# Performance work log

Hardware: AMD Instinct MI355X
Metric: run time of the kernel (lower is better)

## Reference

```python
import jax, jax.numpy as jnp
import numpy as np

N = 50000   # nodes
E = 800000  # edges
IN = 128
HID = 128
L = 4       # GraphConv layers
OUT = 47    # classes
EPS = 1e-5  # BatchNorm eps


def setup_inputs() -> dict:
    key = jax.random.key(0)
    ks = jax.random.split(key, 12)
    feat = jax.random.normal(ks[0], (N, IN), jnp.float32)
    src = jax.random.randint(ks[1], (E,), 0, N, jnp.int32)
    dst = jax.random.randint(ks[2], (E,), 0, N, jnp.int32)
    enc_W = jax.random.normal(ks[3], (L, IN, HID), jnp.float32) * 0.05
    enc_bias = jnp.zeros((HID,), jnp.float32)
    bn_gamma = jnp.ones((L, HID), jnp.float32)
    bn_beta = jnp.zeros((L, HID), jnp.float32)
    bn_mean = jax.random.normal(ks[4], (L, HID), jnp.float32) * 0.1
    bn_var = jnp.ones((L, HID), jnp.float32) + 0.1 * jax.random.uniform(ks[5], (L, HID), jnp.float32)
    cls_W0 = jax.random.normal(ks[6], (HID * L, HID), jnp.float32) * 0.05
    cls_b0 = jnp.zeros((HID,), jnp.float32)
    cls_gamma0 = jnp.ones((HID,), jnp.float32)
    cls_beta0 = jnp.zeros((HID,), jnp.float32)
    cls_mean0 = jax.random.normal(ks[7], (HID,), jnp.float32) * 0.1
    cls_var0 = jnp.ones((HID,), jnp.float32) + 0.1 * jax.random.uniform(ks[8], (HID,), jnp.float32)
    cls_W1 = jax.random.normal(ks[9], (HID, OUT), jnp.float32) * 0.05
    cls_b1 = jnp.zeros((OUT,), jnp.float32)
    return dict(feat=feat, src=src, dst=dst, enc_W=enc_W, enc_bias=enc_bias,
                bn_gamma=bn_gamma, bn_beta=bn_beta, bn_mean=bn_mean, bn_var=bn_var,
                cls_W0=cls_W0, cls_b0=cls_b0, cls_gamma0=cls_gamma0, cls_beta0=cls_beta0,
                cls_mean0=cls_mean0, cls_var0=cls_var0, cls_W1=cls_W1, cls_b1=cls_b1)


def _bn_eval(x, gamma, beta, mean, var):
    return (x - mean) * (gamma * jax.lax.rsqrt(var + EPS)) + beta


def reference(feat, src, dst, enc_W, enc_bias, bn_gamma, bn_beta, bn_mean, bn_var,
              cls_W0, cls_b0, cls_gamma0, cls_beta0, cls_mean0, cls_var0, cls_W1, cls_b1):
    ones = jnp.ones((E,), jnp.float32)
    out_deg = jnp.clip(jax.ops.segment_sum(ones, src, num_segments=N), 1.0)
    in_deg = jnp.clip(jax.ops.segment_sum(ones, dst, num_segments=N), 1.0)
    norm_src = jax.lax.rsqrt(out_deg)[:, None]  # [N,1]
    norm_dst = jax.lax.rsqrt(in_deg)[:, None]

    h = feat  # inference: dropout = identity
    feat_lst = []
    for i in range(L):
        # GraphConv 'both': D_out^{-1/2} pre-scale, XW, scatter-add over edges, D_in^{-1/2} post-scale
        hw = (h * norm_src) @ enc_W[i]                         # [N,HID]
        agg = jax.ops.segment_sum(hw[src], dst, num_segments=N)  # sparse neighbor aggregation
        h = agg * norm_dst
        if i == L - 1:  # only last GraphConv has bias
            h = h + enc_bias
        h = _bn_eval(h, bn_gamma[i], bn_beta[i], bn_mean[i], bn_var[i])
        h = jax.nn.relu(h)
        feat_lst.append(h)

    h = jnp.concatenate(feat_lst, axis=-1)  # JK concat -> [N, HID*L]
    # classifier layer 0: Linear + BN + ReLU (dropout off in eval)
    h = _bn_eval(h @ cls_W0 + cls_b0, cls_gamma0, cls_beta0, cls_mean0, cls_var0)
    h = jax.nn.relu(h)
    # classifier layer 1: Linear only
    return h @ cls_W1 + cls_b1  # [N, OUT]
```

## Files before the change

### kernel.cpp

```cpp
#include <hip/hip_runtime.h>
#include <hip/hip_bf16.h>
#include <hip/hip_fp16.h>

#define EPS 1e-5f
#define HB 128
#define HRANGE 25600
#define NN2 51200

typedef __attribute__((ext_vector_type(8))) short short8;
typedef __attribute__((ext_vector_type(4))) float f32x4;

__device__ __forceinline__ unsigned short f2bf_rn(float f) {
    unsigned u = __builtin_bit_cast(unsigned, f);
    u += 0x7fffu + ((u >> 16) & 1u);
    return (unsigned short)(u >> 16);
}
__device__ __forceinline__ float bf2f(unsigned short h) {
    return __builtin_bit_cast(float, (unsigned)h << 16);
}
__device__ __forceinline__ unsigned packsplit(float x) {
    unsigned short h = f2bf_rn(x);
    unsigned short l = f2bf_rn(x - bf2f(h));
    return ((unsigned)h << 16) | l;
}

__global__ __launch_bounds__(1024) void hist_kernel(
    const int* __restrict__ src, const int* __restrict__ dst,
    unsigned* __restrict__ histW, int E, int EperB) {
    __shared__ unsigned cnt[HRANGE];
    const int b = blockIdx.x, tid = threadIdx.x;
    const long e0 = (long)b * EperB;
    const long e1 = min(e0 + (long)EperB, (long)E);
    #pragma unroll 2
    for (int arr = 0; arr < 2; ++arr) {
        const int* a = arr ? src : dst;
        for (int j = tid; j < HRANGE; j += 1024) cnt[j] = 0;
        __syncthreads();
        for (long e = e0 + tid; e < e1; e += 1024) {
            int v = a[e];
            atomicAdd(&cnt[v >> 1], 1u << ((v & 1) << 4));
        }
        __syncthreads();
        unsigned* o = histW + ((size_t)(arr * HB + b)) * HRANGE;
        for (int j = tid; j < HRANGE; j += 1024) o[j] = cnt[j];
        __syncthreads();
    }
}

__global__ __launch_bounds__(256) void merge_kernel(
    const unsigned short* __restrict__ hist16, int* __restrict__ pdeg,
    unsigned short* __restrict__ bp16, float* __restrict__ nsrc,
    float* __restrict__ ndst, int N) {
    int n = blockIdx.x * blockDim.x + threadIdx.x;
    if (n >= NN2) return;
    unsigned s = 0;
    #pragma unroll 8
    for (int b = 0; b < HB; ++b) {
        unsigned c = hist16[(size_t)b * NN2 + n];
        bp16[(size_t)b * NN2 + n] = (unsigned short)s;
        s += c;
    }
    unsigned s2 = 0;
    #pragma unroll 8
    for (int b = 0; b < HB; ++b) s2 += hist16[(size_t)(HB + b) * NN2 + n];
    if (n < N) {
        pdeg[n] = (int)((s + 15u) & ~15u);
        ndst[n] = rsqrtf((float)max((int)s, 1));
        nsrc[n] = rsqrtf((float)max((int)s2, 1));
    }
}

__global__ __launch_bounds__(256) void scan_partial_kernel(const int* __restrict__ deg,
                                                           int* __restrict__ bsums, int n) {
    __shared__ int wsum[4];
    const int tid = threadIdx.x, lane = tid & 63, wid = tid >> 6;
    const int i0 = blockIdx.x * 1024 + tid * 4;
    int s = 0;
    if (i0 + 3 < n) {
        int4 v = *(const int4*)(deg + i0);
        s = v.x + v.y + v.z + v.w;
    } else {
        for (int j = 0; j < 4; ++j) if (i0 + j < n) s += deg[i0 + j];
    }
    #pragma unroll
    for (int off = 32; off >= 1; off >>= 1) s += __shfl_down(s, off, 64);
    if (lane == 0) wsum[wid] = s;
    __syncthreads();
    if (tid == 0) bsums[blockIdx.x] = wsum[0] + wsum[1] + wsum[2] + wsum[3];
}

__global__ __launch_bounds__(64) void scan_bsums_kernel(int* __restrict__ bsums,
                                                        int* __restrict__ offs, int nb, int n) {
    int lane = threadIdx.x;
    int v = (lane < nb) ? bsums[lane] : 0;
    int x = v;
    #pragma unroll
    for (int off = 1; off < 64; off <<= 1) {
        int t = __shfl_up(x, off, 64);
        if (lane >= off) x += t;
    }
    if (lane < nb) bsums[lane] = x - v;
    if (lane == 63) offs[n] = x;
}

__global__ __launch_bounds__(256) void scan_final_kernel(const int* __restrict__ deg,
                                                         const int* __restrict__ bsums,
                                                         int* __restrict__ offs, int n) {
    __shared__ int wsum[4];
    const int tid = threadIdx.x, lane = tid & 63, wid = tid >> 6;
    const int i0 = blockIdx.x * 1024 + tid * 4;
    int d0 = 0, d1 = 0, d2 = 0, d3 = 0;
    if (i0 + 3 < n) {
        int4 v = *(const int4*)(deg + i0);
        d0 = v.x; d1 = v.y; d2 = v.z; d3 = v.w;
    } else {
        if (i0 + 0 < n) d0 = deg[i0 + 0];
        if (i0 + 1 < n) d1 = deg[i0 + 1];
        if (i0 + 2 < n) d2 = deg[i0 + 2];
        if (i0 + 3 < n) d3 = deg[i0 + 3];
    }
    int s = d0 + d1 + d2 + d3;
    int x = s;
    #pragma unroll
    for (int off = 1; off < 64; off <<= 1) {
        int t = __shfl_up(x, off, 64);
        if (lane >= off) x += t;
    }
    if (lane == 63) wsum[wid] = x;
    __syncthreads();
    int wpre = 0;
    #pragma unroll
    for (int w = 0; w < 4; ++w) if (w < wid) wpre += wsum[w];
    int base = bsums[blockIdx.x] + wpre + (x - s);
    if (i0 + 0 < n) offs[i0 + 0] = base;
    if (i0 + 1 < n) offs[i0 + 1] = base + d0;
    if (i0 + 2 < n) offs[i0 + 2] = base + d0 + d1;
    if (i0 + 3 < n) offs[i0 + 3] = base + d0 + d1 + d2;
}

__global__ void fill_pad_kernel(int* __restrict__ csc, int total, int N) {
    int i = blockIdx.x * blockDim.x + threadIdx.x;
    int o = i * 4;
    if (o + 3 < total) {
        *(int4*)(csc + o) = make_int4(N, N, N, N);
    } else {
        for (int j = 0; j < 4 && o + j < total; ++j) csc[o + j] = N;
    }
}

__global__ __launch_bounds__(1024) void fill_kernel(
    const int* __restrict__ src, const int* __restrict__ dst,
    const int* __restrict__ offs, const unsigned short* __restrict__ bp16,
    int* __restrict__ csc, int E, int EperB) {
    __shared__ unsigned cur[HRANGE];
    const int b = blockIdx.x, tid = threadIdx.x;
    const long e0 = (long)b * EperB;
    const long e1 = min(e0 + (long)EperB, (long)E);
    for (int j = tid; j < HRANGE; j += 1024) cur[j] = 0;
    __syncthreads();
    const unsigned short* bprow = bp16 + (size_t)b * NN2;
    for (long e = e0 + tid; e < e1; e += 1024) {
        int d = dst[e];
        int sh = (d & 1) << 4;
        unsigned old = atomicAdd(&cur[d >> 1], 1u << sh);
        unsigned rank = (old >> sh) & 0xffffu;
        unsigned p = (unsigned)offs[d] + (unsigned)bprow[d] + rank;
        csc[p] = src[e];
    }
}

__device__ __forceinline__ void pack_frag(
    const float* __restrict__ B, short* __restrict__ hi, short* __restrict__ lo,
    int K, int NCF, int strideB, int ncols, int t) {
    int KF = K >> 5;
    int lane = t & 63;
    int fid = t >> 6;
    int cf = fid / KF;
    int kf = fid % KF;
    int col = cf * 16 + (lane & 15);
    int k0 = kf * 32 + (lane >> 4) * 8;
    int o = t * 8;
    #pragma unroll
    for (int j = 0; j < 8; ++j) {
        float x = (col < ncols) ? B[(size_t)(k0 + j) * strideB + col] : 0.f;
        unsigned short h = f2bf_rn(x);
        hi[o + j] = (short)h;
        lo[o + j] = (short)f2bf_rn(x - bf2f(h));
    }
}

__global__ __launch_bounds__(256) void pack_all_kernel(
    const float* __restrict__ enc_W, const float* __restrict__ cls_W0,
    const float* __restrict__ cls_W1,
    short* __restrict__ encBhi, short* __restrict__ encBlo,
    short* __restrict__ clsBhi, short* __restrict__ clsBlo,
    short* __restrict__ w1hi, short* __restrict__ w1lo) {
    int t = blockIdx.x * blockDim.x + threadIdx.x;
    if (t < 8192) {
        int i = t >> 11, tt = t & 2047;
        pack_frag(enc_W + (size_t)i * 128 * 128, encBhi + i * 16384, encBlo + i * 16384,
                  128, 8, 128, 128, tt);
    } else if (t < 16384) {
        pack_frag(cls_W0, clsBhi, clsBlo, 512, 8, 128, 128, t - 8192);
    } else if (t < 16384 + 768) {
        pack_frag(cls_W1, w1hi, w1lo, 128, 3, 47, 47, t - 16384);
    }
}

template<bool PACKED>
__global__ __launch_bounds__(256) void mfma_gemm_kernel(
    const void* __restrict__ Av, const short* __restrict__ Bhi, const short* __restrict__ Blo,
    const float* __restrict__ nsrc, __half* __restrict__ C, int M) {
    __shared__ short Bh_sh[16384];
    __shared__ short Bl_sh[16384];
    const int tid = threadIdx.x;
    const int lane = tid & 63;
    const int wid  = tid >> 6;
    const int row0 = blockIdx.x * 128 + wid * 32;
    const int rsub = lane & 15;
    const int kg   = lane >> 4;

    short8 ahi[2][4], alo[2][4];
    #pragma unroll
    for (int rf = 0; rf < 2; ++rf) {
        const int rowa = min(row0 + rf * 16 + rsub, M - 1);
        #pragma unroll
        for (int kf = 0; kf < 4; ++kf) {
            short8 h, l;
            if (PACKED) {
                const unsigned* ap = (const unsigned*)Av + (size_t)rowa * 128 + kg * 8;
                uint4 u0 = *(const uint4*)(ap + kf * 32);
                uint4 u1 = *(const uint4*)(ap + kf * 32 + 4);
                unsigned uu[8] = {u0.x, u0.y, u0.z, u0.w, u1.x, u1.y, u1.z, u1.w};
                #pragma unroll
                for (int j = 0; j < 8; ++j) {
                    h[j] = (short)(uu[j] >> 16);
                    l[j] = (short)(uu[j] & 0xffffu);
                }
            } else {
                const float* ap = (const float*)Av + (size_t)rowa * 128 + kg * 8;
                float4 v0 = *(const float4*)(ap + kf * 32);
                float4 v1 = *(const float4*)(ap + kf * 32 + 4);
                float v[8] = {v0.x, v0.y, v0.z, v0.w, v1.x, v1.y, v1.z, v1.w};
                #pragma unroll
                for (int j = 0; j < 8; ++j) {
                    unsigned short hb = f2bf_rn(v[j]);
                    h[j] = (short)hb;
                    l[j] = (short)f2bf_rn(v[j] - bf2f(hb));
                }
            }
            ahi[rf][kf] = h; alo[rf][kf] = l;
        }
    }

    #pragma unroll
    for (int i = 0; i < 8; ++i) {
        int o = (tid + i * 256) * 8;
        *(uint4*)&Bh_sh[o] = *(const uint4*)&Bhi[o];
        *(uint4*)&Bl_sh[o] = *(const uint4*)&Blo[o];
    }
    __syncthreads();

    f32x4 acc[2][8];
    #pragma unroll
    for (int rf = 0; rf < 2; ++rf)
        #pragma unroll
        for (int cf = 0; cf < 8; ++cf) acc[rf][cf] = (f32x4){0.f, 0.f, 0.f, 0.f};

    #pragma unroll
    for (int cf = 0; cf < 8; ++cf) {
        #pragma unroll
        for (int kf = 0; kf < 4; ++kf) {
            int o = ((cf * 4 + kf) * 64 + lane) * 8;
            short8 bh = *(const short8*)&Bh_sh[o];
            short8 bl = *(const short8*)&Bl_sh[o];
            #pragma unroll
            for (int rf = 0; rf < 2; ++rf) {
                acc[rf][cf] = __builtin_amdgcn_mfma_f32_16x16x32_bf16(ahi[rf][kf], bh, acc[rf][cf], 0, 0, 0);
                acc[rf][cf] = __builtin_amdgcn_mfma_f32_16x16x32_bf16(alo[rf][kf], bh, acc[rf][cf], 0, 0, 0);
                acc[rf][cf] = __builtin_amdgcn_mfma_f32_16x16x32_bf16(ahi[rf][kf], bl, acc[rf][cf], 0, 0, 0);
            }
        }
    }

    #pragma unroll
    for (int rf = 0; rf < 2; ++rf)
        #pragma unroll
        for (int r = 0; r < 4; ++r) {
            int row = row0 + rf * 16 + kg * 4 + r;
            if (row < M) {
                float sc = nsrc[row];
                __half* cp = C + (size_t)row * 128 + rsub;
                #pragma unroll
                for (int cf = 0; cf < 8; ++cf) cp[cf * 16] = __float2half(acc[rf][cf][r] * sc);
            }
        }
}

__global__ __launch_bounds__(256) void aggregate_kernel(
    const __half* __restrict__ hw, const int* __restrict__ offs, const int* __restrict__ csc,
    const float* __restrict__ norm_dst, const float* __restrict__ bias,
    const float* __restrict__ gamma, const float* __restrict__ beta,
    const float* __restrict__ mean, const float* __restrict__ var,
    unsigned* __restrict__ hout, int n) {
    const int lane = threadIdx.x & 63;
    const int gw = (blockIdx.x * blockDim.x + threadIdx.x) >> 6;
    const int nw = (gridDim.x * blockDim.x) >> 6;
    const int c = lane * 2;

    const float sc0 = gamma[c] * rsqrtf(var[c] + EPS);
    const float sc1 = gamma[c + 1] * rsqrtf(var[c + 1] + EPS);
    const float mn0 = mean[c], mn1 = mean[c + 1];
    const float bt0 = beta[c], bt1 = beta[c + 1];
    const float bi0 = bias ? bias[c] : 0.f;
    const float bi1 = bias ? bias[c + 1] : 0.f;

    for (int v = gw; v < n; v += nw) {
        const int e0 = offs[v], e1 = offs[v + 1];
        float2 acc = make_float2(0.f, 0.f);
        for (int e = e0; e < e1; e += 16) {
            int4 ca = *(const int4*)(csc + e);
            int4 cb = *(const int4*)(csc + e + 4);
            int4 cc = *(const int4*)(csc + e + 8);
            int4 cd = *(const int4*)(csc + e + 12);
            float2 p0 = __half22float2(*(const __half2*)(hw + (size_t)ca.x * 128 + c));
            float2 p1 = __half22float2(*(const __half2*)(hw + (size_t)ca.y * 128 + c));
            float2 p2 = __half22float2(*(const __half2*)(hw + (size_t)ca.z * 128 + c));
            float2 p3 = __half22float2(*(const __half2*)(hw + (size_t)ca.w * 128 + c));
            float2 p4 = __half22float2(*(const __half2*)(hw + (size_t)cb.x * 128 + c));
            float2 p5 = __half22float2(*(const __half2*)(hw + (size_t)cb.y * 128 + c));
            float2 p6 = __half22float2(*(const __half2*)(hw + (size_t)cb.z * 128 + c));
            float2 p7 = __half22float2(*(const __half2*)(hw + (size_t)cb.w * 128 + c));
            float2 p8 = __half22float2(*(const __half2*)(hw + (size_t)cc.x * 128 + c));
            float2 p9 = __half22float2(*(const __half2*)(hw + (size_t)cc.y * 128 + c));
            float2 pa = __half22float2(*(const __half2*)(hw + (size_t)cc.z * 128 + c));
            float2 pb = __half22float2(*(const __half2*)(hw + (size_t)cc.w * 128 + c));
            float2 pc = __half22float2(*(const __half2*)(hw + (size_t)cd.x * 128 + c));
            float2 pd = __half22float2(*(const __half2*)(hw + (size_t)cd.y * 128 + c));
            float2 pe = __half22float2(*(const __half2*)(hw + (size_t)cd.z * 128 + c));
            float2 pf = __half22float2(*(const __half2*)(hw + (size_t)cd.w * 128 + c));
            acc.x += (((p0.x + p1.x) + (p2.x + p3.x)) + ((p4.x + p5.x) + (p6.x + p7.x)))
                   + (((p8.x + p9.x) + (pa.x + pb.x)) + ((pc.x + pd.x) + (pe.x + pf.x)));
            acc.y += (((p0.y + p1.y) + (p2.y + p3.y)) + ((p4.y + p5.y) + (p6.y + p7.y)))
                   + (((p8.y + p9.y) + (pa.y + pb.y)) + ((pc.y + pd.y) + (pe.y + pf.y)));
        }
        float nd = norm_dst[v];
        float h0 = fmaxf((acc.x * nd + bi0 - mn0) * sc0 + bt0, 0.f);
        float h1 = fmaxf((acc.y * nd + bi1 - mn1) * sc1 + bt1, 0.f);
        uint2 w = make_uint2(packsplit(h0), packsplit(h1));
        *(uint2*)(hout + (size_t)v * 128 + c) = w;
    }
}

__global__ __launch_bounds__(256) void classifier_kernel(
    const unsigned* __restrict__ h1, const unsigned* __restrict__ h2,
    const unsigned* __restrict__ h3, const unsigned* __restrict__ h4,
    const short* __restrict__ Bhi, const short* __restrict__ Blo,
    const short* __restrict__ W1hi, const short* __restrict__ W1lo,
    const float* __restrict__ b0,
    const float* __restrict__ g, const float* __restrict__ bt,
    const float* __restrict__ mn, const float* __restrict__ vr,
    const float* __restrict__ b1,
    float* __restrict__ out, int M) {
    __shared__ short Bh_sh[2][4096];
    __shared__ short Bl_sh[2][4096];
    __shared__ unsigned zw[4][16 * 128];
    const int tid = threadIdx.x, lane = tid & 63, wid = tid >> 6;
    const int rsub = lane & 15;
    const int kg   = lane >> 4;
    const int row0 = blockIdx.x * 128 + wid * 32;
    const unsigned* hb[4] = {h1, h2, h3, h4};

    const int scf = tid >> 5, ssub = tid & 31;
    const int sl = scf * 512 + ssub * 16;

    float biasv[8], scalev[8], meanv[8], betav[8];
    #pragma unroll
    for (int cf = 0; cf < 8; ++cf) {
        int col = cf * 16 + rsub;
        biasv[cf] = b0[col];
        scalev[cf] = g[col] * rsqrtf(vr[col] + EPS);
        meanv[cf] = mn[col];
        betav[cf] = bt[col];
    }

    f32x4 acc[2][8];
    #pragma unroll
    for (int rf = 0; rf < 2; ++rf)
        #pragma unroll
        for (int cf = 0; cf < 8; ++cf) acc[rf][cf] = (f32x4){0.f, 0.f, 0.f, 0.f};

    {
        size_t goff = ((size_t)(scf * 16 + 0) * 64) * 8 + ssub * 16;
        *(uint4*)&Bh_sh[0][sl]     = *(const uint4*)&Bhi[goff];
        *(uint4*)&Bh_sh[0][sl + 8] = *(const uint4*)&Bhi[goff + 8];
        *(uint4*)&Bl_sh[0][sl]     = *(const uint4*)&Blo[goff];
        *(uint4*)&Bl_sh[0][sl + 8] = *(const uint4*)&Blo[goff + 8];
    }
    __syncthreads();

    const int rowa0 = min(row0 + rsub, M - 1);
    const int rowa1 = min(row0 + 16 + rsub, M - 1);

    for (int kf16 = 0; kf16 < 16; ++kf16) {
        const int cur = kf16 & 1;
        uint4 st0, st1, st2, st3;
        if (kf16 < 15) {
            size_t goff = ((size_t)(scf * 16 + kf16 + 1) * 64) * 8 + ssub * 16;
            st0 = *(const uint4*)&Bhi[goff];
            st1 = *(const uint4*)&Bhi[goff + 8];
            st2 = *(const uint4*)&Blo[goff];
            st3 = *(const uint4*)&Blo[goff + 8];
        }
        short8 ah[2], al[2];
        #pragma unroll
        for (int rf = 0; rf < 2; ++rf) {
            const unsigned* ap = hb[kf16 >> 2] + (size_t)(rf ? rowa1 : rowa0) * 128
                                 + (kf16 & 3) * 32 + kg * 8;
            uint4 u0 = *(const uint4*)(ap);
            uint4 u1 = *(const uint4*)(ap + 4);
            unsigned uu[8] = {u0.x, u0.y, u0.z, u0.w, u1.x, u1.y, u1.z, u1.w};
            #pragma unroll
            for (int j = 0; j < 8; ++j) {
                ah[rf][j] = (short)(uu[j] >> 16);
                al[rf][j] = (short)(uu[j] & 0xffffu);
            }
        }
        #pragma unroll
        for (int cf = 0; cf < 8; ++cf) {
            int o = (cf * 64 + lane) * 8;
            short8 bh = *(const short8*)&Bh_sh[cur][o];
            short8 bl = *(const short8*)&Bl_sh[cur][o];
            #pragma unroll
            for (int rf = 0; rf < 2; ++rf) {
                acc[rf][cf] = __builtin_amdgcn_mfma_f32_16x16x32_bf16(ah[rf], bh, acc[rf][cf], 0, 0, 0);
                acc[rf][cf] = __builtin_amdgcn_mfma_f32_16x16x32_bf16(al[rf], bh, acc[rf][cf], 0, 0, 0);
                acc[rf][cf] = __builtin_amdgcn_mfma_f32_16x16x32_bf16(ah[rf], bl, acc[rf][cf], 0, 0, 0);
            }
        }
        if (kf16 < 15) {
            *(uint4*)&Bh_sh[cur ^ 1][sl]     = st0;
            *(uint4*)&Bh_sh[cur ^ 1][sl + 8] = st1;
            *(uint4*)&Bl_sh[cur ^ 1][sl]     = st2;
            *(uint4*)&Bl_sh[cur ^ 1][sl + 8] = st3;
        }
        __syncthreads();
    }

    f32x4 oacc[2][3];
    #pragma unroll
    for (int rf = 0; rf < 2; ++rf)
        #pragma unroll
        for (int cf = 0; cf < 3; ++cf) oacc[rf][cf] = (f32x4){0.f, 0.f, 0.f, 0.f};

    #pragma unroll
    for (int rf = 0; rf < 2; ++rf) {
        #pragma unroll
        for (int cf = 0; cf < 8; ++cf) {
            int col = cf * 16 + rsub;
            #pragma unroll
            for (int r = 0; r < 4; ++r) {
                int rloc = kg * 4 + r;
                float z = fmaxf((acc[rf][cf][r] + biasv[cf] - meanv[cf]) * scalev[cf] + betav[cf], 0.f);
                zw[wid][rloc * 128 + (col ^ ((rloc & 7) << 2))] = packsplit(z);
            }
        }
        const int rloc = rsub;
        const int sw = (rloc & 7) << 2;
        #pragma unroll
        for (int kf = 0; kf < 4; ++kf) {
            int k0 = kf * 32 + kg * 8;
            uint4 ua = *(const uint4*)&zw[wid][rloc * 128 + (k0 ^ sw)];
            uint4 ub = *(const uint4*)&zw[wid][rloc * 128 + ((k0 + 4) ^ sw)];
            unsigned uu[8] = {ua.x, ua.y, ua.z, ua.w, ub.x, ub.y, ub.z, ub.w};
            short8 zh, zl;
            #pragma unroll
            for (int j = 0; j < 8; ++j) {
                zh[j] = (short)(uu[j] >> 16);
                zl[j] = (short)(uu[j] & 0xffffu);
            }
            #pragma unroll
            for (int cf = 0; cf < 3; ++cf) {
                int bidx = ((cf * 4 + kf) * 64 + lane) * 8;
                short8 wh = *(const short8*)(W1hi + bidx);
                short8 wl = *(const short8*)(W1lo + bidx);
                oacc[rf][cf] = __builtin_amdgcn_mfma_f32_16x16x32_bf16(zh, wh, oacc[rf][cf], 0, 0, 0);
                oacc[rf][cf] = __builtin_amdgcn_mfma_f32_16x16x32_bf16(zl, wh, oacc[rf][cf], 0, 0, 0);
                oacc[rf][cf] = __builtin_amdgcn_mfma_f32_16x16x32_bf16(zh, wl, oacc[rf][cf], 0, 0, 0);
            }
        }
    }

    #pragma unroll
    for (int rf = 0; rf < 2; ++rf)
        #pragma unroll
        for (int cf = 0; cf < 3; ++cf) {
            int col = cf * 16 + rsub;
            if (col < 47) {
                float bb = b1[col];
                #pragma unroll
                for (int r = 0; r < 4; ++r) {
                    int row = row0 + rf * 16 + kg * 4 + r;
                    if (row < M) out[(size_t)row * 47 + col] = oacc[rf][cf][r] + bb;
                }
            }
        }
}

extern "C" void kernel_launch(void* const* d_in, const int* in_sizes, int n_in,
                              void* d_out, int out_size, void* d_ws, size_t ws_size,
                              hipStream_t stream) {
    const float* feat     = (const float*)d_in[0];
    const int*   src      = (const int*)d_in[1];
    const int*   dst      = (const int*)d_in[2];
    const float* enc_W    = (const float*)d_in[3];
    const float* enc_bias = (const float*)d_in[4];
    const float* bn_gamma = (const float*)d_in[5];
    const float* bn_beta  = (const float*)d_in[6];
    const float* bn_mean  = (const float*)d_in[7];
    const float* bn_var   = (const float*)d_in[8];
    const float* cls_W0   = (const float*)d_in[9];
    const float* cls_b0   = (const float*)d_in[10];
    const float* cls_g0   = (const float*)d_in[11];
    const float* cls_be0  = (const float*)d_in[12];
    const float* cls_m0   = (const float*)d_in[13];
    const float* cls_v0   = (const float*)d_in[14];
    const float* cls_W1   = (const float*)d_in[15];
    const float* cls_b1   = (const float*)d_in[16];
    float* out = (float*)d_out;

    const int N_ = in_sizes[0] / 128;
    const int E_ = in_sizes[1];
    const int cscCap = E_ + 15 * N_ + 64;

    char* p = (char*)d_ws;
    auto alloc = [&](size_t bytes) {
        char* r = p;
        p += (bytes + 255) & ~(size_t)255;
        return r;
    };
    __half* h_b = (__half*)alloc((size_t)(N_ + 1) * 128 * 2);
    unsigned* hl[4];
    for (int i = 0; i < 4; ++i) hl[i] = (unsigned*)alloc((size_t)N_ * 128 * 4);
    float* norm_src = (float*)alloc((size_t)NN2 * 4);
    float* norm_dst = (float*)alloc((size_t)NN2 * 4);
    int* pdeg   = (int*)alloc((size_t)NN2 * 4);
    int* offs   = (int*)alloc((size_t)(N_ + 1) * 4);
    int* csc    = (int*)alloc((size_t)cscCap * 4);
    int* bsums  = (int*)alloc(256 * 4);
    unsigned* histW = (unsigned*)alloc((size_t)2 * HB * HRANGE * 4);
    unsigned short* bp16 = (unsigned short*)alloc((size_t)HB * NN2 * 2);
    short* encBhi = (short*)alloc(4 * 16384 * 2);
    short* encBlo = (short*)alloc(4 * 16384 * 2);
    short* clsBhi = (short*)alloc(65536 * 2);
    short* clsBlo = (short*)alloc(65536 * 2);
    short* w1hi   = (short*)alloc(6144 * 2);
    short* w1lo   = (short*)alloc(6144 * 2);

    const int EperB = (E_ + HB - 1) / HB;
    const int nb = (N_ + 1023) / 1024;

    hipMemsetAsync(h_b + (size_t)N_ * 128, 0, 256, stream);

    hist_kernel<<<HB, 1024, 0, stream>>>(src, dst, histW, E_, EperB);
    merge_kernel<<<(NN2 + 255) / 256, 256, 0, stream>>>(
        (const unsigned short*)histW, pdeg, bp16, norm_src, norm_dst, N_);
    scan_partial_kernel<<<nb, 256, 0, stream>>>(pdeg, bsums, N_);
    scan_bsums_kernel<<<1, 64, 0, stream>>>(bsums, offs, nb, N_);
    scan_final_kernel<<<nb, 256, 0, stream>>>(pdeg, bsums, offs, N_);
    fill_pad_kernel<<<(cscCap / 4 + 255) / 256, 256, 0, stream>>>(csc, cscCap, N_);
    fill_kernel<<<HB, 1024, 0, stream>>>(src, dst, offs, bp16, csc, E_, EperB);

    pack_all_kernel<<<(16384 + 768 + 255) / 256, 256, 0, stream>>>(
        enc_W, cls_W0, cls_W1, encBhi, encBlo, clsBhi, clsBlo, w1hi, w1lo);

    const int gblocks = (N_ + 127) / 128;
    const int agg_blocks = (N_ + 3) / 4;

    for (int i = 0; i < 4; ++i) {
        if (i == 0)
            mfma_gemm_kernel<false><<<gblocks, 256, 0, stream>>>(
                feat, encBhi, encBlo, norm_src, h_b, N_);
        else
            mfma_gemm_kernel<true><<<gblocks, 256, 0, stream>>>(
                hl[i - 1], encBhi + i * 16384, encBlo + i * 16384, norm_src, h_b, N_);
        aggregate_kernel<<<agg_blocks, 256, 0, stream>>>(
            h_b, offs, csc, norm_dst,
            (i == 3) ? enc_bias : nullptr,
            bn_gamma + i * 128, bn_beta + i * 128, bn_mean + i * 128, bn_var + i * 128,
            hl[i], N_);
    }
    classifier_kernel<<<gblocks, 256, 0, stream>>>(
        hl[0], hl[1], hl[2], hl[3], clsBhi, clsBlo, w1hi, w1lo, cls_b0,
        cls_g0, cls_be0, cls_m0, cls_v0, cls_b1, out, N_);
}
```

Measured before the change: 305.5 us.

## Split histogram across two block sets and aggregate two nodes per wavefront

The histogram kernel now launches twice as many blocks, with each block handling either src or dst instead of looping over both. The aggregate kernel has each half-wavefront (32 lanes × 4 columns) process one destination node. Each lane issues 8-byte gathers and a 16-byte store, and per-node edge padding drops from 16 to 8. Together these cut the padding gathers wasted on low-degree nodes and raise parallelism in the histogram. The trade-off is fewer lanes per node row and more blocks competing for the large shared-memory histogram.

```diff
diff --git a/kernel.cpp b/kernel.cpp
--- a/kernel.cpp
+++ b/kernel.cpp
@@ -28,23 +28,22 @@
     const int* __restrict__ src, const int* __restrict__ dst,
     unsigned* __restrict__ histW, int E, int EperB) {
     __shared__ unsigned cnt[HRANGE];
-    const int b = blockIdx.x, tid = threadIdx.x;
+    const int bb = blockIdx.x;
+    const int arr = (bb >= HB) ? 1 : 0;
+    const int b = arr ? (bb - HB) : bb;
+    const int tid = threadIdx.x;
+    const int* a = arr ? src : dst;
     const long e0 = (long)b * EperB;
     const long e1 = min(e0 + (long)EperB, (long)E);
-    #pragma unroll 2
-    for (int arr = 0; arr < 2; ++arr) {
-        const int* a = arr ? src : dst;
-        for (int j = tid; j < HRANGE; j += 1024) cnt[j] = 0;
-        __syncthreads();
-        for (long e = e0 + tid; e < e1; e += 1024) {
-            int v = a[e];
-            atomicAdd(&cnt[v >> 1], 1u << ((v & 1) << 4));
-        }
-        __syncthreads();
-        unsigned* o = histW + ((size_t)(arr * HB + b)) * HRANGE;
-        for (int j = tid; j < HRANGE; j += 1024) o[j] = cnt[j];
-        __syncthreads();
-    }
+    for (int j = tid; j < HRANGE; j += 1024) cnt[j] = 0;
+    __syncthreads();
+    for (long e = e0 + tid; e < e1; e += 1024) {
+        int v = a[e];
+        atomicAdd(&cnt[v >> 1], 1u << ((v & 1) << 4));
+    }
+    __syncthreads();
+    unsigned* o = histW + ((size_t)(arr * HB + b)) * HRANGE;
+    for (int j = tid; j < HRANGE; j += 1024) o[j] = cnt[j];
 }
 
 __global__ __launch_bounds__(256) void merge_kernel(
@@ -64,7 +63,7 @@
     #pragma unroll 8
     for (int b = 0; b < HB; ++b) s2 += hist16[(size_t)(HB + b) * NN2 + n];
     if (n < N) {
-        pdeg[n] = (int)((s + 15u) & ~15u);
+        pdeg[n] = (int)((s + 7u) & ~7u);
         ndst[n] = rsqrtf((float)max((int)s, 1));
         nsrc[n] = rsqrtf((float)max((int)s2, 1));
     }
@@ -304,51 +303,65 @@
     const float* __restrict__ mean, const float* __restrict__ var,
     unsigned* __restrict__ hout, int n) {
     const int lane = threadIdx.x & 63;
+    const int half = lane >> 5;
+    const int c = (lane & 31) * 4;
     const int gw = (blockIdx.x * blockDim.x + threadIdx.x) >> 6;
     const int nw = (gridDim.x * blockDim.x) >> 6;
-    const int c = lane * 2;
-
-    const float sc0 = gamma[c] * rsqrtf(var[c] + EPS);
-    const float sc1 = gamma[c + 1] * rsqrtf(var[c + 1] + EPS);
-    const float mn0 = mean[c], mn1 = mean[c + 1];
-    const float bt0 = beta[c], bt1 = beta[c + 1];
-    const float bi0 = bias ? bias[c] : 0.f;
-    const float bi1 = bias ? bias[c + 1] : 0.f;
-
-    for (int v = gw; v < n; v += nw) {
+
+    float scv[4], mnv[4], btv[4], biv[4];
+    #pragma unroll
+    for (int j = 0; j < 4; ++j) {
+        int col = c + j;
+        scv[j] = gamma[col] * rsqrtf(var[col] + EPS);
+        mnv[j] = mean[col];
+        btv[j] = beta[col];
+        biv[j] = bias ? bias[col] : 0.f;
+    }
+
+    for (int vb = gw * 2; vb < n; vb += nw * 2) {
+        const int v = min(vb + half, n - 1);
         const int e0 = offs[v], e1 = offs[v + 1];
-        float2 acc = make_float2(0.f, 0.f);
-        for (int e = e0; e < e1; e += 16) {
+        float4 acc = make_float4(0.f, 0.f, 0.f, 0.f);
+        for (int e = e0; e < e1; e += 8) {
             int4 ca = *(const int4*)(csc + e);
             int4 cb = *(const int4*)(csc + e + 4);
-            int4 cc = *(const int4*)(csc + e + 8);
-            int4 cd = *(const int4*)(csc + e + 12);
-            float2 p0 = __half22float2(*(const __half2*)(hw + (size_t)ca.x * 128 + c));
-            float2 p1 = __half22float2(*(const __half2*)(hw + (size_t)ca.y * 128 + c));
-            float2 p2 = __half22float2(*(const __half2*)(hw + (size_t)ca.z * 128 + c));
-            float2 p3 = __half22float2(*(const __half2*)(hw + (size_t)ca.w * 128 + c));
-            float2 p4 = __half22float2(*(const __half2*)(hw + (size_t)cb.x * 128 + c));
-            float2 p5 = __half22float2(*(const __half2*)(hw + (size_t)cb.y * 128 + c));
-            float2 p6 = __half22float2(*(const __half2*)(hw + (size_t)cb.z * 128 + c));
-            float2 p7 = __half22float2(*(const __half2*)(hw + (size_t)cb.w * 128 + c));
-            float2 p8 = __half22float2(*(const __half2*)(hw + (size_t)cc.x * 128 + c));
-            float2 p9 = __half22float2(*(const __half2*)(hw + (size_t)cc.y * 128 + c));
-            float2 pa = __half22float2(*(const __half2*)(hw + (size_t)cc.z * 128 + c));
-            float2 pb = __half22float2(*(const __half2*)(hw + (size_t)cc.w * 128 + c));
-            float2 pc = __half22float2(*(const __half2*)(hw + (size_t)cd.x * 128 + c));
-            float2 pd = __half22float2(*(const __half2*)(hw + (size_t)cd.y * 128 + c));
-            float2 pe = __half22float2(*(const __half2*)(hw + (size_t)cd.z * 128 + c));
-            float2 pf = __half22float2(*(const __half2*)(hw + (size_t)cd.w * 128 + c));
-            acc.x += (((p0.x + p1.x) + (p2.x + p3.x)) + ((p4.x + p5.x) + (p6.x + p7.x)))
-                   + (((p8.x + p9.x) + (pa.x + pb.x)) + ((pc.x + pd.x) + (pe.x + pf.x)));
-            acc.y += (((p0.y + p1.y) + (p2.y + p3.y)) + ((p4.y + p5.y) + (p6.y + p7.y)))
-                   + (((p8.y + p9.y) + (pa.y + pb.y)) + ((pc.y + pd.y) + (pe.y + pf.y)));
+            uint2 u0 = *(const uint2*)(hw + (size_t)ca.x * 128 + c);
+            uint2 u1 = *(const uint2*)(hw + (size_t)ca.y * 128 + c);
+            uint2 u2 = *(const uint2*)(hw + (size_t)ca.z * 128 + c);
+            uint2 u3 = *(const uint2*)(hw + (size_t)ca.w * 128 + c);
+            uint2 u4 = *(const uint2*)(hw + (size_t)cb.x * 128 + c);
+            uint2 u5 = *(const uint2*)(hw + (size_t)cb.y * 128 + c);
+            uint2 u6 = *(const uint2*)(hw + (size_t)cb.z * 128 + c);
+            uint2 u7 = *(const uint2*)(hw + (size_t)cb.w * 128 + c);
+            uint2 uu[8] = {u0, u1, u2, u3, u4, u5, u6, u7};
+            float4 a0 = make_float4(0.f, 0.f, 0.f, 0.f);
+            float4 a1 = make_float4(0.f, 0.f, 0.f, 0.f);
+            #pragma unroll
+            for (int j = 0; j < 8; j += 2) {
+                float2 fa = __half22float2(__builtin_bit_cast(__half2, uu[j].x));
+                float2 fb = __half22float2(__builtin_bit_cast(__half2, uu[j].y));
+                float2 ga = __half22float2(__builtin_bit_cast(__half2, uu[j + 1].x));
+                float2 gb = __half22float2(__builtin_bit_cast(__half2, uu[j + 1].y));
+                a0.x += fa.x; a0.y += fa.y; a0.z += fb.x; a0.w += fb.y;
+                a1.x += ga.x; a1.y += ga.y; a1.z += gb.x; a1.w += gb.y;
+            }
+            acc.x += a0.x + a1.x;
+            acc.y += a0.y + a1.y;
+            acc.z += a0.z + a1.z;
+            acc.w += a0.w + a1.w;
         }
         float nd = norm_dst[v];
-        float h0 = fmaxf((acc.x * nd + bi0 - mn0) * sc0 + bt0, 0.f);
-        float h1 = fmaxf((acc.y * nd + bi1 - mn1) * sc1 + bt1, 0.f);
-        uint2 w = make_uint2(packsplit(h0), packsplit(h1));
-        *(uint2*)(hout + (size_t)v * 128 + c) = w;
+        float av[4] = {acc.x, acc.y, acc.z, acc.w};
+        uint4 w;
+        unsigned wv[4];
+        #pragma unroll
+        for (int j = 0; j < 4; ++j) {
+            float h = fmaxf((av[j] * nd + biv[j] - mnv[j]) * scv[j] + btv[j], 0.f);
+            wv[j] = packsplit(h);
+        }
+        w = make_uint4(wv[0], wv[1], wv[2], wv[3]);
+        if (vb + half < n)
+            *(uint4*)(hout + (size_t)v * 128 + c) = w;
     }
 }
 
@@ -531,7 +544,7 @@
 
     const int N_ = in_sizes[0] / 128;
     const int E_ = in_sizes[1];
-    const int cscCap = E_ + 15 * N_ + 64;
+    const int cscCap = E_ + 7 * N_ + 64;
 
     char* p = (char*)d_ws;
     auto alloc = [&](size_t bytes) {
@@ -562,7 +575,7 @@
 
     hipMemsetAsync(h_b + (size_t)N_ * 128, 0, 256, stream);
 
-    hist_kernel<<<HB, 1024, 0, stream>>>(src, dst, histW, E_, EperB);
+    hist_kernel<<<2 * HB, 1024, 0, stream>>>(src, dst, histW, E_, EperB);
     merge_kernel<<<(NN2 + 255) / 256, 256, 0, stream>>>(
         (const unsigned short*)histW, pdeg, bp16, norm_src, norm_dst, N_);
     scan_partial_kernel<<<nb, 256, 0, stream>>>(pdeg, bsums, N_);
@@ -575,7 +588,7 @@
         enc_W, cls_W0, cls_W1, encBhi, encBlo, clsBhi, clsBlo, w1hi, w1lo);
 
     const int gblocks = (N_ + 127) / 128;
-    const int agg_blocks = (N_ + 3) / 4;
+    const int agg_blocks = (N_ + 7) / 8;
 
     for (int i = 0; i < 4; ++i) {
         if (i == 0)
```

After: 360.1 us. 17.9% more time.
